# Kernel optimization log

Measured on AMD Instinct MI355X. Metric: run time of the kernel, lower is better.

Reference implementation:

```python
import jax, jax.numpy as jnp
import numpy as np

N = 13627
E = 504378
D = 500


def _seg_softmax(e, seg, n):
    m = jax.ops.segment_max(e, seg, num_segments=n)
    ex = jnp.exp(e - m[seg])
    s = jax.ops.segment_sum(ex, seg, num_segments=n)
    return ex / (s[seg] + 1e-16)


def _gatv2(x, src, dst, Wl, Wr, att, b, n):
    # PyG GATv2Conv (heads=1): message = Wl x_src; score uses Wl x_src + Wr x_dst
    xl = x @ Wl                                   # [N, F]
    xr = x @ Wr                                   # [N, F]
    e = jax.nn.leaky_relu(xl[src] + xr[dst], 0.2) @ att   # [E]
    a = _seg_softmax(e, dst, n)                   # segment softmax over targets
    out = jax.ops.segment_sum(a[:, None] * xl[src], dst, num_segments=n)
    return out + b


def setup_inputs() -> dict:
    key = jax.random.key(0)
    ks = jax.random.split(key, 24)
    s = 0.05
    inp = {
        'x': jax.random.normal(ks[0], (N, D), dtype=jnp.float32),
        'edge_index': jax.random.randint(ks[1], (2, E), 0, N),
        'neg_edge_index': jax.random.randint(ks[2], (2, E), 0, N),
        'Wl1': jax.random.normal(ks[3], (D, 300)) * s,
        'Wr1': jax.random.normal(ks[4], (D, 300)) * s,
        'att1': jax.random.normal(ks[5], (300,)) * s,
        'b1': jnp.zeros((300,)),
        'Wl2': jax.random.normal(ks[6], (300, 100)) * s,
        'Wr2': jax.random.normal(ks[7], (300, 100)) * s,
        'att2': jax.random.normal(ks[8], (100,)) * s,
        'b2': jnp.zeros((100,)),
        'Wl3': jax.random.normal(ks[9], (100, 1)) * s,
        'Wr3': jax.random.normal(ks[10], (100, 1)) * s,
        'att3': jax.random.normal(ks[11], (1,)) * s,
        'b3': jnp.zeros((1,)),
        'W_lin1': jax.random.normal(ks[12], (D, 100)) * s,
        'b_lin1': jnp.zeros((100,)),
        'W_lin2': jax.random.normal(ks[13], (D, 100)) * s,
        'b_lin2': jnp.zeros((100,)),
        'c1': jnp.array([0.5], dtype=jnp.float32),
        'c2': jnp.array([0.5], dtype=jnp.float32),
    }
    return inp


def reference(x, edge_index, neg_edge_index, Wl1, Wr1, att1, b1, Wl2, Wr2, att2, b2,
              Wl3, Wr3, att3, b3, W_lin1, b_lin1, W_lin2, b_lin2, c1, c2):
    # eval mode: dropout / dropout_adj are identity
    loops = jnp.arange(N)
    src = jnp.concatenate([edge_index[0], loops])   # GATv2Conv adds self loops
    dst = jnp.concatenate([edge_index[1], loops])

    h1 = jax.nn.relu(_gatv2(x, src, dst, Wl1, Wr1, att1, b1, N))
    h2 = jax.nn.relu(_gatv2(h1, src, dst, Wl2, Wr2, att2, b2, N))

    xo = h2 + jax.nn.relu(x @ W_lin1 + b_lin1)
    z = h2 + jax.nn.relu(x @ W_lin2 + b_lin2)

    # link-prediction reconstruction loss
    pos_s = jnp.sum(z[edge_index[0]] * z[edge_index[1]], axis=1)
    pos_loss = -jnp.mean(jnp.log(jax.nn.sigmoid(pos_s) + 1e-15))
    neg_s = jnp.sum(z[neg_edge_index[0]] * z[neg_edge_index[1]], axis=1)
    neg_loss = -jnp.mean(jnp.log(1.0 - jax.nn.sigmoid(neg_s) + 1e-15))
    r_loss = pos_loss + neg_loss

    out = _gatv2(xo, src, dst, Wl3, Wr3, att3, b3, N)   # [N, 1]
    return out, r_loss, c1, c2
```

## Files before the change

kernel.cpp:

```cpp
#include <hip/hip_runtime.h>
#include <hip/hip_bf16.h>

#define NODES 13627
#define DIM   500

typedef short short8 __attribute__((ext_vector_type(8)));
typedef float f32x4 __attribute__((ext_vector_type(4)));
typedef float floatx2 __attribute__((ext_vector_type(2)));

__device__ inline float wave_reduce_sum(float v) {
#pragma unroll
    for (int o = 32; o > 0; o >>= 1) v += __shfl_xor(v, o, 64);
    return v;
}

__device__ inline void store_v(float* p, float v) { *p = v; }
__device__ inline void store_v(__hip_bfloat16* p, float v) { *p = __float2bfloat16(v); }

__device__ inline float blo(unsigned w) { unsigned t = w << 16;        return __builtin_bit_cast(float, t); }
__device__ inline float bhi(unsigned w) { unsigned t = w & 0xffff0000u; return __builtin_bit_cast(float, t); }

__device__ inline unsigned char to_fp8(float v) {
    int r = __builtin_amdgcn_cvt_pk_fp8_f32(v, v, 0, false);
    return (unsigned char)(r & 0xff);
}

__device__ inline unsigned pk2bf(float a, float b) {
    unsigned la = (unsigned)__builtin_bit_cast(unsigned short, __float2bfloat16(a));
    unsigned hb = (unsigned)__builtin_bit_cast(unsigned short, __float2bfloat16(b));
    return la | (hb << 16);
}

struct b4 { __hip_bfloat16 a, b, c, d; };

__global__ __launch_bounds__(256) void hist_kernel(const int* __restrict__ dst,
                                                   int* __restrict__ cnt, int E) {
    int i = blockIdx.x * blockDim.x + threadIdx.x;
    if (i < E) atomicAdd(&cnt[dst[i]], 1);
}

__global__ __launch_bounds__(1024) void scan_kernel(int* __restrict__ cnt_cur,
                                                    int* __restrict__ off, int n) {
    __shared__ int wsum[16];
    const int tid = threadIdx.x, lane = tid & 63, w = tid >> 6;
    int carry = 0;
    for (int base = 0; base < n; base += 1024) {
        int i = base + tid;
        int v = (i < n) ? cnt_cur[i] : 0;
        int s = v;
#pragma unroll
        for (int o = 1; o < 64; o <<= 1) {
            int t = __shfl_up(s, o, 64);
            if (lane >= o) s += t;
        }
        if (lane == 63) wsum[w] = s;
        __syncthreads();
        if (w == 0 && lane < 16) {
            int x = wsum[lane];
            int sx = x;
#pragma unroll
            for (int o = 1; o < 16; o <<= 1) {
                int t = __shfl_up(sx, o, 64);
                if (lane >= o) sx += t;
            }
            wsum[lane] = sx;
        }
        __syncthreads();
        int wo = (w == 0) ? 0 : wsum[w - 1];
        int total = wsum[15];
        int excl = carry + wo + (s - v);
        if (i < n) { off[i] = excl; cnt_cur[i] = excl; }
        carry += total;
        __syncthreads();
    }
    if (tid == 0) off[n] = carry;
}

__global__ __launch_bounds__(256) void scatter_kernel(const int* __restrict__ src,
                                                      const int* __restrict__ dst,
                                                      int* __restrict__ cur,
                                                      int* __restrict__ ssrc, int E) {
    int i = blockIdx.x * blockDim.x + threadIdx.x;
    if (i < E) {
        int p = atomicAdd(&cur[dst[i]], 1);
        ssrc[p] = src[i];
    }
}

__global__ __launch_bounds__(256) void convert_all_kernel(
    const float* __restrict__ x,
    const float* __restrict__ Wl1, const float* __restrict__ Wr1,
    const float* __restrict__ Wl2, const float* __restrict__ Wr2,
    const float* __restrict__ Ws1, const float* __restrict__ Ws2,
    const float* __restrict__ bs1, const float* __restrict__ bs2,
    __hip_bfloat16* __restrict__ W1T, __hip_bfloat16* __restrict__ W2T,
    __hip_bfloat16* __restrict__ WsT, float* __restrict__ bcat,
    __hip_bfloat16* __restrict__ xb, int M) {
    int i = blockIdx.x * 256 + threadIdx.x;
    if (i < 327680) {
        int n = i >> 9, k = i & 511;
        float v = 0.f;
        if (k < 500) {
            if (n < 300) v = Wl1[k * 300 + n];
            else if (n < 600) v = Wr1[k * 300 + n - 300];
        }
        W1T[i] = __float2bfloat16(v);
    } else if (i < 409600) {
        int j = i - 327680;
        int n = j / 320, k = j - n * 320;
        float v = 0.f;
        if (k < 300) {
            if (n < 100) v = Wl2[k * 100 + n];
            else if (n < 200) v = Wr2[k * 100 + n - 100];
        }
        W2T[j] = __float2bfloat16(v);
    } else if (i < 540672) {
        int j = i - 409600;
        int n = j >> 9, k = j & 511;
        float v = 0.f;
        if (k < 500) {
            if (n < 100) v = Ws1[k * 100 + n];
            else if (n < 200) v = Ws2[k * 100 + n - 100];
        }
        WsT[j] = __float2bfloat16(v);
    } else if (i < 540928) {
        int n = i - 540672;
        float v = 0.f;
        if (n < 100) v = bs1[n];
        else if (n < 200) v = bs2[n - 100];
        bcat[n] = v;
    } else {
        int j = i - 540928;
        if (j >= M * 128) return;
        int m = j >> 7, k = (j & 127) << 2;
        b4 o;
        if (k < 500) {
            float4 v = *(const float4*)(x + (size_t)m * 500 + k);
            o.a = __float2bfloat16(v.x); o.b = __float2bfloat16(v.y);
            o.c = __float2bfloat16(v.z); o.d = __float2bfloat16(v.w);
        } else {
            o.a = o.b = o.c = o.d = __float2bfloat16(0.f);
        }
        *(b4*)(xb + (size_t)m * 512 + k) = o;
    }
}

template <int EPI, typename TC>
__global__ __launch_bounds__(256) void mfma_gemm(
    const __hip_bfloat16* __restrict__ A, const __hip_bfloat16* __restrict__ BT,
    TC* __restrict__ C, const float* __restrict__ bias, const float* __restrict__ h2,
    unsigned char* __restrict__ p8, __hip_bfloat16* __restrict__ pb,
    int M, int Kp, int Nn, int ldc) {
    __shared__ short AsF[8 * 64 * 8];
    __shared__ short BsF[4 * 64 * 8];
    const int t = threadIdx.x;
    const int w = t >> 6, lane = t & 63;
    const int c = t & 3, rr = t >> 2;
    const int m0 = blockIdx.y * 128, n0 = blockIdx.x * 64;

    f32x4 acc[2][4];
#pragma unroll
    for (int i = 0; i < 2; i++)
#pragma unroll
        for (int j = 0; j < 4; j++) acc[i][j] = (f32x4){0.f, 0.f, 0.f, 0.f};

    for (int k0 = 0; k0 < Kp; k0 += 32) {
#pragma unroll
        for (int r = 0; r < 2; r++) {
            int m = r * 64 + rr;
            int gm = m0 + m; if (gm >= M) gm = M - 1;
            float4 v = *(const float4*)(A + (size_t)gm * Kp + k0 + c * 8);
            int mi = m >> 4, sl = m & 15;
            *(float4*)(&AsF[(mi * 64 + c * 16 + sl) * 8]) = v;
        }
        {
            int n = rr;
            float4 v = *(const float4*)(BT + (size_t)(n0 + n) * Kp + k0 + c * 8);
            int ni = n >> 4, sl = n & 15;
            *(float4*)(&BsF[(ni * 64 + c * 16 + sl) * 8]) = v;
        }
        __syncthreads();
        short8 a0 = *(const short8*)(&AsF[((w * 2 + 0) * 64 + lane) * 8]);
        short8 a1 = *(const short8*)(&AsF[((w * 2 + 1) * 64 + lane) * 8]);
#pragma unroll
        for (int j = 0; j < 4; j++) {
            short8 b = *(const short8*)(&BsF[(j * 64 + lane) * 8]);
            acc[0][j] = __builtin_amdgcn_mfma_f32_16x16x32_bf16(a0, b, acc[0][j], 0, 0, 0);
            acc[1][j] = __builtin_amdgcn_mfma_f32_16x16x32_bf16(a1, b, acc[1][j], 0, 0, 0);
        }
        __syncthreads();
    }

    const int q = lane >> 4, sl = lane & 15;
#pragma unroll
    for (int i = 0; i < 2; i++) {
#pragma unroll
        for (int j = 0; j < 4; j++) {
#pragma unroll
            for (int reg = 0; reg < 4; reg++) {
                int gm = m0 + w * 32 + i * 16 + q * 4 + reg;
                int gn = n0 + j * 16 + sl;
                if (gm >= M) continue;
                float v = acc[i][j][reg];
                if constexpr (EPI == 1) {
                    if (gn < 300)       p8[(size_t)gm * 304 + gn] = to_fp8(v);
                    else if (gn < 600)  pb[(size_t)gm * 320 + (gn - 300)] = __float2bfloat16(v);
                    else if (gn < 620)  pb[(size_t)gm * 320 + (gn - 300)] = __float2bfloat16(0.f);
                    else if (gn < 624)  p8[(size_t)gm * 304 + (gn - 320)] = 0;
                } else if constexpr (EPI == 2) {
                    if (gn < 100)       p8[(size_t)gm * 112 + gn] = to_fp8(v);
                    else if (gn < 200)  pb[(size_t)gm * 128 + (gn - 100)] = __float2bfloat16(v);
                    else if (gn < 212)  p8[(size_t)gm * 112 + (gn - 100)] = 0;
                    else if (gn < 240)  pb[(size_t)gm * 128 + (gn - 112)] = __float2bfloat16(0.f);
                } else if constexpr (EPI == 3) {
                    if (gn < 200) {
                        int cn = gn < 100 ? gn : gn - 100;
                        float val = fmaxf(v + bias[gn], 0.f) + h2[(size_t)gm * 100 + cn];
                        if (gn < 100) C[(size_t)gm * 100 + gn] = val;
                        else p8[(size_t)gm * 128 + (gn - 100)] = to_fp8(val);
                    } else if (gn < 228) {
                        p8[(size_t)gm * 128 + (gn - 100)] = 0;
                    }
                } else {
                    store_v(&C[(size_t)gm * ldc + gn], v);
                }
            }
        }
    }
}

template <int F, int SL8, int SRB>
__global__ __launch_bounds__(256) void attdot_kernel(
    const unsigned char* __restrict__ xl8, const __hip_bfloat16* __restrict__ xrb,
    const float* __restrict__ att, float* __restrict__ sxl, float* __restrict__ sxr,
    int n) {
    const int wid = blockIdx.x * 4 + (threadIdx.x >> 6);
    const int lane = threadIdx.x & 63;
    if (wid >= n) return;
    float al = 0.f, ar = 0.f;
    for (int f0 = lane * 4; f0 < F; f0 += 256) {
        float4 a = *(const float4*)(att + f0);
        unsigned u = *(const unsigned*)(xl8 + (size_t)wid * SL8 + f0);
        floatx2 lo = __builtin_amdgcn_cvt_pk_f32_fp8((int)u, false);
        floatx2 hi = __builtin_amdgcn_cvt_pk_f32_fp8((int)u, true);
        al += a.x * lo.x + a.y * lo.y + a.z * hi.x + a.w * hi.y;
        uint2 r = *(const uint2*)(xrb + (size_t)wid * SRB + f0);
        ar += a.x * blo(r.x) + a.y * bhi(r.x) + a.z * blo(r.y) + a.w * bhi(r.y);
    }
    al = wave_reduce_sum(al);
    ar = wave_reduce_sum(ar);
    if (lane == 0) { sxl[wid] = 0.6f * al; sxr[wid] = 0.6f * ar; }
}

template <int F, int NJ, int SL8, int SRB, int SOUT, int JSL, typename TOUT>
__global__ __launch_bounds__(256) void gat_f8_kernel(
    const unsigned char* __restrict__ xl8, const __hip_bfloat16* __restrict__ xrb,
    const float* __restrict__ att, const float* __restrict__ bias,
    const float* __restrict__ sxl, const float* __restrict__ sxr,
    const int* __restrict__ off, const int* __restrict__ ssrc,
    TOUT* __restrict__ out, int n) {
    __shared__ float sden[2];
    __shared__ float sacc[2][NJ * 64];
    const int t = threadIdx.x;
    const int lane = t & 63;
    const int sl = lane & 15, q = lane >> 4;
    const int half = (t >> 6) & 1;
    const int pairIdx = t >> 7;
    int wid = blockIdx.x * 2 + pairIdx;
    if (wid >= n) wid = n - 1;

    float att4[NJ * 4], xrv[NJ * 4], acc[NJ * 4];
    const unsigned* xru = (const unsigned*)xrb + (size_t)wid * (SRB / 2);
#pragma unroll
    for (int j = 0; j < NJ; j++) {
        const int f0 = sl * 4 + j * 64;
        if (f0 < F) {
            float4 a4 = *(const float4*)(att + f0);
            att4[j * 4 + 0] = 0.4f * a4.x; att4[j * 4 + 1] = 0.4f * a4.y;
            att4[j * 4 + 2] = 0.4f * a4.z; att4[j * 4 + 3] = 0.4f * a4.w;
        } else {
            att4[j * 4 + 0] = att4[j * 4 + 1] = att4[j * 4 + 2] = att4[j * 4 + 3] = 0.f;
        }
        unsigned u0 = __builtin_nontemporal_load(xru + (f0 >> 1));
        unsigned u1 = __builtin_nontemporal_load(xru + (f0 >> 1) + 1);
        xrv[j * 4 + 0] = blo(u0); xrv[j * 4 + 1] = bhi(u0);
        xrv[j * 4 + 2] = blo(u1); xrv[j * 4 + 3] = bhi(u1);
        acc[j * 4 + 0] = acc[j * 4 + 1] = acc[j * 4 + 2] = acc[j * 4 + 3] = 0.f;
    }
    const float pbase = sxr[wid];

    const int s0 = off[wid], s1 = off[wid + 1];
    const int h0 = (s1 - s0) >> 1;
    const int eb = half ? (s0 + h0) : (s0 - 1);
    const int ee = half ? s1 : (s0 + h0);
    float den = 0.f;

    for (int e0 = eb; e0 < ee; e0 += 4) {
        const int eq = e0 + q;
        const bool act = eq < ee;
        int src = wid;
        if (act && eq >= s0) src = __builtin_nontemporal_load(ssrc + eq);
        const unsigned char* row = xl8 + (size_t)src * SL8;
        unsigned u[NJ];
#pragma unroll
        for (int j = 0; j < NJ; j++) {
            const bool ld = (j < NJ - 1) || (sl < JSL);
            u[j] = ld ? *(const unsigned*)(row + sl * 4 + j * 64) : 0u;
        }
        float xlv[NJ * 4];
        float p = (sl == 0) ? (pbase + sxl[src]) : 0.f;
#pragma unroll
        for (int j = 0; j < NJ; j++) {
            floatx2 lo = __builtin_amdgcn_cvt_pk_f32_fp8((int)u[j], false);
            floatx2 hi = __builtin_amdgcn_cvt_pk_f32_fp8((int)u[j], true);
            float v[4] = {lo.x, lo.y, hi.x, hi.y};
#pragma unroll
            for (int cc = 0; cc < 4; cc++) {
                xlv[j * 4 + cc] = v[cc];
                float s = v[cc] + xrv[j * 4 + cc];
                p = fmaf(att4[j * 4 + cc], fabsf(s), p);
            }
        }
        p += __shfl_xor(p, 1, 64);
        p += __shfl_xor(p, 2, 64);
        p += __shfl_xor(p, 4, 64);
        p += __shfl_xor(p, 8, 64);
        float ex = act ? expf(p) : 0.f;
        den += ex;
#pragma unroll
        for (int i = 0; i < NJ * 4; i++) acc[i] += ex * xlv[i];
    }

#pragma unroll
    for (int o = 16; o <= 32; o <<= 1) {
        den += __shfl_xor(den, o, 64);
#pragma unroll
        for (int i = 0; i < NJ * 4; i++) acc[i] += __shfl_xor(acc[i], o, 64);
    }

    if (half == 1 && lane < 16) {
        if (lane == 0) sden[pairIdx] = den;
#pragma unroll
        for (int j = 0; j < NJ; j++)
            *(float4*)(&sacc[pairIdx][sl * 4 + j * 64]) =
                make_float4(acc[j * 4 + 0], acc[j * 4 + 1], acc[j * 4 + 2], acc[j * 4 + 3]);
    }
    __syncthreads();
    if (half == 0 && lane < 16) {
        den += sden[pairIdx];
        const float inv = 1.f / (den + 1e-16f);
#pragma unroll
        for (int j = 0; j < NJ; j++) {
            const int f0 = sl * 4 + j * 64;
            if (f0 >= SOUT) continue;
            float4 o4 = *(float4*)(&sacc[pairIdx][f0]);
            float vv[4] = {acc[j * 4 + 0] + o4.x, acc[j * 4 + 1] + o4.y,
                           acc[j * 4 + 2] + o4.z, acc[j * 4 + 3] + o4.w};
            float r[4];
#pragma unroll
            for (int cc = 0; cc < 4; cc++) {
                const int f = f0 + cc;
                float v = 0.f;
                if (f < F) v = fmaxf(vv[cc] * inv + bias[f], 0.f);
                r[cc] = v;
            }
            if constexpr (sizeof(TOUT) == 4) {
                float* op = (float*)out + (size_t)wid * SOUT + f0;
                __builtin_nontemporal_store(r[0], op + 0);
                __builtin_nontemporal_store(r[1], op + 1);
                __builtin_nontemporal_store(r[2], op + 2);
                __builtin_nontemporal_store(r[3], op + 3);
            } else {
                unsigned* op = (unsigned*)out + (size_t)wid * (SOUT / 2) + (f0 >> 1);
                __builtin_nontemporal_store(pk2bf(r[0], r[1]), op);
                __builtin_nontemporal_store(pk2bf(r[2], r[3]), op + 1);
            }
        }
    }
}

__global__ __launch_bounds__(256) void gemm_vec1_kernel(
    const float* __restrict__ xo, const float* __restrict__ wl,
    const float* __restrict__ wr, float* __restrict__ xl3,
    float* __restrict__ xr3, int M, int ldx) {
    const int wid = blockIdx.x * 4 + (threadIdx.x >> 6);
    const int lane = threadIdx.x & 63;
    if (wid >= M) return;
    float a = 0.f, b = 0.f;
    for (int f = lane; f < 100; f += 64) {
        float v = xo[(size_t)wid * ldx + f];
        a += v * wl[f];
        b += v * wr[f];
    }
    a = wave_reduce_sum(a);
    b = wave_reduce_sum(b);
    if (lane == 0) { xl3[wid] = a; xr3[wid] = b; }
}

__global__ __launch_bounds__(256) void gat3_kernel(
    const float* __restrict__ xl3, const float* __restrict__ xr3,
    const float* __restrict__ att3, const float* __restrict__ b3,
    const int* __restrict__ off, const int* __restrict__ ssrc,
    float* __restrict__ out, int n) {
    const int wid = blockIdx.x * 4 + (threadIdx.x >> 6);
    const int lane = threadIdx.x & 63;
    if (wid >= n) return;
    const float xrv = xr3[wid];
    const float att = att3[0];
    float num = 0.f, den = 0.f;
    const int s0 = off[wid], s1 = off[wid + 1];
    for (int e = s0 - 1 + lane; e < s1; e += 64) {
        int src = (e < s0) ? wid : ssrc[e];
        float xlv = xl3[src];
        float t = xlv + xrv;
        float g = t > 0.f ? t : 0.2f * t;
        float ex = expf(g * att);
        den += ex;
        num += ex * xlv;
    }
    num = wave_reduce_sum(num);
    den = wave_reduce_sum(den);
    if (lane == 0) out[wid] = num / (den + 1e-16f) + b3[0];
}

__global__ __launch_bounds__(256) void loss_kernel(
    const unsigned char* __restrict__ z8, const int* __restrict__ pos,
    const int* __restrict__ neg, float* __restrict__ part, int nb, int E) {
    const int lane = threadIdx.x & 63;
    const int sl = lane & 15;
    const int wlocal = threadIdx.x >> 6;
    const int q = lane >> 4;
    const int nq = gridDim.x * 16;
    const int qid = (blockIdx.x * 4 + wlocal) * 4 + q;
    const int total = 2 * E;
    float psum = 0.f, nsum = 0.f;

    for (int base = qid; base < total; base += 4 * nq) {
        uint2 au[4], bu[4];
        bool act[4], isN[4];
#pragma unroll
        for (int s = 0; s < 4; s++) {
            int it = base + s * nq;
            act[s] = it < total;
            int itc = act[s] ? it : 0;
            isN[s] = itc >= E;
            int e = isN[s] ? itc - E : itc;
            const int* ei = isN[s] ? neg : pos;
            int u = ei[e], v = ei[E + e];
            au[s] = *(const uint2*)(z8 + (size_t)u * 128 + sl * 8);
            bu[s] = *(const uint2*)(z8 + (size_t)v * 128 + sl * 8);
        }
#pragma unroll
        for (int s = 0; s < 4; s++) {
            floatx2 a0 = __builtin_amdgcn_cvt_pk_f32_fp8((int)au[s].x, false);
            floatx2 a1 = __builtin_amdgcn_cvt_pk_f32_fp8((int)au[s].x, true);
            floatx2 a2 = __builtin_amdgcn_cvt_pk_f32_fp8((int)au[s].y, false);
            floatx2 a3 = __builtin_amdgcn_cvt_pk_f32_fp8((int)au[s].y, true);
            floatx2 b0 = __builtin_amdgcn_cvt_pk_f32_fp8((int)bu[s].x, false);
            floatx2 b1 = __builtin_amdgcn_cvt_pk_f32_fp8((int)bu[s].x, true);
            floatx2 b2 = __builtin_amdgcn_cvt_pk_f32_fp8((int)bu[s].y, false);
            floatx2 b3 = __builtin_amdgcn_cvt_pk_f32_fp8((int)bu[s].y, true);
            float p = a0.x * b0.x + a0.y * b0.y + a1.x * b1.x + a1.y * b1.y
                    + a2.x * b2.x + a2.y * b2.y + a3.x * b3.x + a3.y * b3.y;
            p += __shfl_xor(p, 1, 64);
            p += __shfl_xor(p, 2, 64);
            p += __shfl_xor(p, 4, 64);
            p += __shfl_xor(p, 8, 64);
            if (sl == 0 && act[s]) {
                float sig = 1.f / (1.f + expf(-p));
                if (isN[s]) nsum += logf(1.f - sig + 1e-15f);
                else        psum += logf(sig + 1e-15f);
            }
        }
    }
    float pw = wave_reduce_sum(psum);
    float nw = wave_reduce_sum(nsum);
    __shared__ float sp[4], sn[4];
    if (lane == 0) { sp[wlocal] = pw; sn[wlocal] = nw; }
    __syncthreads();
    if (threadIdx.x == 0) {
        part[blockIdx.x]      = sp[0] + sp[1] + sp[2] + sp[3];
        part[nb + blockIdx.x] = sn[0] + sn[1] + sn[2] + sn[3];
    }
}

__global__ __launch_bounds__(1024) void finalize_kernel(
    const float* __restrict__ part, int nb,
    const float* __restrict__ c1, const float* __restrict__ c2,
    float* __restrict__ out, int n, int E) {
    __shared__ float sp[16], sn[16];
    const int tid = threadIdx.x, lane = tid & 63, w = tid >> 6;
    float p = 0.f, q = 0.f;
    for (int i = tid; i < nb; i += 1024) { p += part[i]; q += part[nb + i]; }
    p = wave_reduce_sum(p);
    q = wave_reduce_sum(q);
    if (lane == 0) { sp[w] = p; sn[w] = q; }
    __syncthreads();
    if (tid == 0) {
        float tp = 0.f, tq = 0.f;
#pragma unroll
        for (int i = 0; i < 16; i++) { tp += sp[i]; tq += sn[i]; }
        out[n]     = -(tp + tq) / (float)E;
        out[n + 1] = c1[0];
        out[n + 2] = c2[0];
    }
}

extern "C" void kernel_launch(void* const* d_in, const int* in_sizes, int n_in,
                              void* d_out, int out_size, void* d_ws, size_t ws_size,
                              hipStream_t stream) {
    const float* x      = (const float*)d_in[0];
    const int*   ei     = (const int*)d_in[1];
    const int*   nei    = (const int*)d_in[2];
    const float* Wl1    = (const float*)d_in[3];
    const float* Wr1    = (const float*)d_in[4];
    const float* att1   = (const float*)d_in[5];
    const float* b1     = (const float*)d_in[6];
    const float* Wl2    = (const float*)d_in[7];
    const float* Wr2    = (const float*)d_in[8];
    const float* att2   = (const float*)d_in[9];
    const float* b2     = (const float*)d_in[10];
    const float* Wl3    = (const float*)d_in[11];
    const float* Wr3    = (const float*)d_in[12];
    const float* att3   = (const float*)d_in[13];
    const float* b3     = (const float*)d_in[14];
    const float* Wlin1  = (const float*)d_in[15];
    const float* blin1  = (const float*)d_in[16];
    const float* Wlin2  = (const float*)d_in[17];
    const float* blin2  = (const float*)d_in[18];
    const float* c1     = (const float*)d_in[19];
    const float* c2     = (const float*)d_in[20];
    float* out = (float*)d_out;

    const int E = in_sizes[1] / 2;
    const int N = NODES;
    const int LOSS_BLOCKS = 4096;

    char* ws = (char*)d_ws;
    unsigned char*  xl8  = (unsigned char*)(ws + 0);
    unsigned char*  xl28 = (unsigned char*)(ws + 0);
    __hip_bfloat16* xrb  = (__hip_bfloat16*)(ws + 4194304);
    __hip_bfloat16* xr2b = (__hip_bfloat16*)(ws + 4194304);
    float*          xo   = (float*)(ws + 4194304);
    unsigned char*  z8   = (unsigned char*)(ws + 9645312);
    __hip_bfloat16* h1b  = (__hip_bfloat16*)(ws + 12915712);
    float*          h2   = (float*)(ws + 12915712);
    __hip_bfloat16* xb   = (__hip_bfloat16*)(ws + 21637120);
    __hip_bfloat16* W1T  = (__hip_bfloat16*)(ws + 35591168);
    __hip_bfloat16* W2T  = (__hip_bfloat16*)(ws + 36246528);
    __hip_bfloat16* WsT  = (__hip_bfloat16*)(ws + 36410368);
    float*          bcat = (float*)(ws + 36672512);
    float*          xl3  = (float*)(ws + 36673536);
    float*          xr3  = (float*)(ws + 36728064);
    int*            ioff = (int*)(ws + 36782592);
    int*            cur  = (int*)(ws + 36837376);
    int*            ssrc = (int*)(ws + 36892160);
    float*          part = (float*)(ws + 38909952);
    float*          sxl  = (float*)(ws + 38942720);
    float*          sxr  = (float*)(ws + 38997248);

    hipMemsetAsync(cur, 0, sizeof(int) * N, stream);

    hist_kernel<<<(E + 255) / 256, 256, 0, stream>>>(ei + E, cur, E);
    scan_kernel<<<1, 1024, 0, stream>>>(cur, ioff, N);
    scatter_kernel<<<(E + 255) / 256, 256, 0, stream>>>(ei, ei + E, cur, ssrc, E);

    convert_all_kernel<<<(540928 + N * 128 + 255) / 256, 256, 0, stream>>>(
        x, Wl1, Wr1, Wl2, Wr2, Wlin1, Wlin2, blin1, blin2,
        W1T, W2T, WsT, bcat, xb, N);

    mfma_gemm<1, __hip_bfloat16><<<dim3(10, 107), 256, 0, stream>>>(
        xb, W1T, (__hip_bfloat16*)nullptr, nullptr, nullptr, xl8, xrb, N, 512, 640, 0);
    attdot_kernel<300, 304, 320><<<(N + 3) / 4, 256, 0, stream>>>(
        xl8, xrb, att1, sxl, sxr, N);
    gat_f8_kernel<300, 5, 304, 320, 320, 11, __hip_bfloat16>
        <<<(N + 1) / 2, 256, 0, stream>>>(xl8, xrb, att1, b1, sxl, sxr, ioff, ssrc, h1b, N);

    mfma_gemm<2, __hip_bfloat16><<<dim3(4, 107), 256, 0, stream>>>(
        h1b, W2T, (__hip_bfloat16*)nullptr, nullptr, nullptr, xl28, xr2b, N, 320, 256, 0);
    attdot_kernel<100, 112, 128><<<(N + 3) / 4, 256, 0, stream>>>(
        xl28, xr2b, att2, sxl, sxr, N);
    gat_f8_kernel<100, 2, 112, 128, 100, 9, float>
        <<<(N + 1) / 2, 256, 0, stream>>>(xl28, xr2b, att2, b2, sxl, sxr, ioff, ssrc, h2, N);

    mfma_gemm<3, float><<<dim3(4, 107), 256, 0, stream>>>(
        xb, WsT, xo, bcat, h2, z8, nullptr, N, 512, 256, 0);

    loss_kernel<<<LOSS_BLOCKS, 256, 0, stream>>>(z8, ei, nei, part, LOSS_BLOCKS, E);

    gemm_vec1_kernel<<<(N + 3) / 4, 256, 0, stream>>>(xo, Wl3, Wr3, xl3, xr3, N, 100);
    gat3_kernel<<<(N + 3) / 4, 256, 0, stream>>>(xl3, xr3, att3, b3, ioff, ssrc, out, N);

    finalize_kernel<<<1, 1024, 0, stream>>>(part, LOSS_BLOCKS, c1, c2, out, N, E);
}
```

Measured before the change: 408.3 us.

## Drop attdot precompute, compute leaky-relu directly, and prefetch next edge rows in GAT

Removes the two attdot kernels. Before, leaky_relu was split into a linear part (0.6·att·x, precomputed per node) plus 0.4·att·|s|. Now the full leaky_relu is evaluated in-loop with fmax(s, 0.2s), which saves two launches and the per-edge sxl gather. The edge loop is software-pipelined: the next group's source index and fp8 row are loaded before the current one is processed, to hide gather latency. The cost is more registers per thread. Nontemporal output stores become plain or vectorised stores.

```diff
diff --git a/kernel.cpp b/kernel.cpp
--- a/kernel.cpp
+++ b/kernel.cpp
@@ -229,34 +229,10 @@
     }
 }
 
-template <int F, int SL8, int SRB>
-__global__ __launch_bounds__(256) void attdot_kernel(
-    const unsigned char* __restrict__ xl8, const __hip_bfloat16* __restrict__ xrb,
-    const float* __restrict__ att, float* __restrict__ sxl, float* __restrict__ sxr,
-    int n) {
-    const int wid = blockIdx.x * 4 + (threadIdx.x >> 6);
-    const int lane = threadIdx.x & 63;
-    if (wid >= n) return;
-    float al = 0.f, ar = 0.f;
-    for (int f0 = lane * 4; f0 < F; f0 += 256) {
-        float4 a = *(const float4*)(att + f0);
-        unsigned u = *(const unsigned*)(xl8 + (size_t)wid * SL8 + f0);
-        floatx2 lo = __builtin_amdgcn_cvt_pk_f32_fp8((int)u, false);
-        floatx2 hi = __builtin_amdgcn_cvt_pk_f32_fp8((int)u, true);
-        al += a.x * lo.x + a.y * lo.y + a.z * hi.x + a.w * hi.y;
-        uint2 r = *(const uint2*)(xrb + (size_t)wid * SRB + f0);
-        ar += a.x * blo(r.x) + a.y * bhi(r.x) + a.z * blo(r.y) + a.w * bhi(r.y);
-    }
-    al = wave_reduce_sum(al);
-    ar = wave_reduce_sum(ar);
-    if (lane == 0) { sxl[wid] = 0.6f * al; sxr[wid] = 0.6f * ar; }
-}
-
 template <int F, int NJ, int SL8, int SRB, int SOUT, int JSL, typename TOUT>
 __global__ __launch_bounds__(256) void gat_f8_kernel(
     const unsigned char* __restrict__ xl8, const __hip_bfloat16* __restrict__ xrb,
     const float* __restrict__ att, const float* __restrict__ bias,
-    const float* __restrict__ sxl, const float* __restrict__ sxr,
     const int* __restrict__ off, const int* __restrict__ ssrc,
     TOUT* __restrict__ out, int n) {
     __shared__ float sden[2];
@@ -269,17 +245,17 @@
     int wid = blockIdx.x * 2 + pairIdx;
     if (wid >= n) wid = n - 1;
 
-    float att4[NJ * 4], xrv[NJ * 4], acc[NJ * 4];
+    float attv[NJ * 4], xrv[NJ * 4], acc[NJ * 4];
     const unsigned* xru = (const unsigned*)xrb + (size_t)wid * (SRB / 2);
 #pragma unroll
     for (int j = 0; j < NJ; j++) {
         const int f0 = sl * 4 + j * 64;
         if (f0 < F) {
             float4 a4 = *(const float4*)(att + f0);
-            att4[j * 4 + 0] = 0.4f * a4.x; att4[j * 4 + 1] = 0.4f * a4.y;
-            att4[j * 4 + 2] = 0.4f * a4.z; att4[j * 4 + 3] = 0.4f * a4.w;
+            attv[j * 4 + 0] = a4.x; attv[j * 4 + 1] = a4.y;
+            attv[j * 4 + 2] = a4.z; attv[j * 4 + 3] = a4.w;
         } else {
-            att4[j * 4 + 0] = att4[j * 4 + 1] = att4[j * 4 + 2] = att4[j * 4 + 3] = 0.f;
+            attv[j * 4 + 0] = attv[j * 4 + 1] = attv[j * 4 + 2] = attv[j * 4 + 3] = 0.f;
         }
         unsigned u0 = __builtin_nontemporal_load(xru + (f0 >> 1));
         unsigned u1 = __builtin_nontemporal_load(xru + (f0 >> 1) + 1);
@@ -287,7 +263,6 @@
         xrv[j * 4 + 2] = blo(u1); xrv[j * 4 + 3] = bhi(u1);
         acc[j * 4 + 0] = acc[j * 4 + 1] = acc[j * 4 + 2] = acc[j * 4 + 3] = 0.f;
     }
-    const float pbase = sxr[wid];
 
     const int s0 = off[wid], s1 = off[wid + 1];
     const int h0 = (s1 - s0) >> 1;
@@ -295,20 +270,35 @@
     const int ee = half ? s1 : (s0 + h0);
     float den = 0.f;
 
-    for (int e0 = eb; e0 < ee; e0 += 4) {
-        const int eq = e0 + q;
-        const bool act = eq < ee;
+    unsigned u[NJ];
+    {
+        int eq = eb + q;
         int src = wid;
-        if (act && eq >= s0) src = __builtin_nontemporal_load(ssrc + eq);
+        if (eq >= s0 && eq < ee) src = __builtin_nontemporal_load(ssrc + eq);
         const unsigned char* row = xl8 + (size_t)src * SL8;
-        unsigned u[NJ];
 #pragma unroll
         for (int j = 0; j < NJ; j++) {
             const bool ld = (j < NJ - 1) || (sl < JSL);
             u[j] = ld ? *(const unsigned*)(row + sl * 4 + j * 64) : 0u;
         }
+    }
+
+    for (int e0 = eb; e0 < ee; e0 += 4) {
+        const bool act = (e0 + q) < ee;
+        unsigned un[NJ];
+        {
+            int eq1 = e0 + 4 + q;
+            int src1 = wid;
+            if (eq1 >= s0 && eq1 < ee) src1 = __builtin_nontemporal_load(ssrc + eq1);
+            const unsigned char* row1 = xl8 + (size_t)src1 * SL8;
+#pragma unroll
+            for (int j = 0; j < NJ; j++) {
+                const bool ld = (j < NJ - 1) || (sl < JSL);
+                un[j] = ld ? *(const unsigned*)(row1 + sl * 4 + j * 64) : 0u;
+            }
+        }
         float xlv[NJ * 4];
-        float p = (sl == 0) ? (pbase + sxl[src]) : 0.f;
+        float p = 0.f;
 #pragma unroll
         for (int j = 0; j < NJ; j++) {
             floatx2 lo = __builtin_amdgcn_cvt_pk_f32_fp8((int)u[j], false);
@@ -318,7 +308,7 @@
             for (int cc = 0; cc < 4; cc++) {
                 xlv[j * 4 + cc] = v[cc];
                 float s = v[cc] + xrv[j * 4 + cc];
-                p = fmaf(att4[j * 4 + cc], fabsf(s), p);
+                p += attv[j * 4 + cc] * fmaxf(s, 0.2f * s);
             }
         }
         p += __shfl_xor(p, 1, 64);
@@ -329,6 +319,8 @@
         den += ex;
 #pragma unroll
         for (int i = 0; i < NJ * 4; i++) acc[i] += ex * xlv[i];
+#pragma unroll
+        for (int j = 0; j < NJ; j++) u[j] = un[j];
     }
 
 #pragma unroll
@@ -365,15 +357,12 @@
                 r[cc] = v;
             }
             if constexpr (sizeof(TOUT) == 4) {
-                float* op = (float*)out + (size_t)wid * SOUT + f0;
-                __builtin_nontemporal_store(r[0], op + 0);
-                __builtin_nontemporal_store(r[1], op + 1);
-                __builtin_nontemporal_store(r[2], op + 2);
-                __builtin_nontemporal_store(r[3], op + 3);
+                *(float4*)((float*)out + (size_t)wid * SOUT + f0) =
+                    make_float4(r[0], r[1], r[2], r[3]);
             } else {
                 unsigned* op = (unsigned*)out + (size_t)wid * (SOUT / 2) + (f0 >> 1);
-                __builtin_nontemporal_store(pk2bf(r[0], r[1]), op);
-                __builtin_nontemporal_store(pk2bf(r[2], r[3]), op + 1);
+                op[0] = pk2bf(r[0], r[1]);
+                op[1] = pk2bf(r[2], r[3]);
             }
         }
     }
@@ -556,8 +545,6 @@
     int*            cur  = (int*)(ws + 36837376);
     int*            ssrc = (int*)(ws + 36892160);
     float*          part = (float*)(ws + 38909952);
-    float*          sxl  = (float*)(ws + 38942720);
-    float*          sxr  = (float*)(ws + 38997248);
 
     hipMemsetAsync(cur, 0, sizeof(int) * N, stream);
 
@@ -571,17 +558,13 @@
 
     mfma_gemm<1, __hip_bfloat16><<<dim3(10, 107), 256, 0, stream>>>(
         xb, W1T, (__hip_bfloat16*)nullptr, nullptr, nullptr, xl8, xrb, N, 512, 640, 0);
-    attdot_kernel<300, 304, 320><<<(N + 3) / 4, 256, 0, stream>>>(
-        xl8, xrb, att1, sxl, sxr, N);
     gat_f8_kernel<300, 5, 304, 320, 320, 11, __hip_bfloat16>
-        <<<(N + 1) / 2, 256, 0, stream>>>(xl8, xrb, att1, b1, sxl, sxr, ioff, ssrc, h1b, N);
+        <<<(N + 1) / 2, 256, 0, stream>>>(xl8, xrb, att1, b1, ioff, ssrc, h1b, N);
 
     mfma_gemm<2, __hip_bfloat16><<<dim3(4, 107), 256, 0, stream>>>(
         h1b, W2T, (__hip_bfloat16*)nullptr, nullptr, nullptr, xl28, xr2b, N, 320, 256, 0);
-    attdot_kernel<100, 112, 128><<<(N + 3) / 4, 256, 0, stream>>>(
-        xl28, xr2b, att2, sxl, sxr, N);
     gat_f8_kernel<100, 2, 112, 128, 100, 9, float>
-        <<<(N + 1) / 2, 256, 0, stream>>>(xl28, xr2b, att2, b2, sxl, sxr, ioff, ssrc, h2, N);
+        <<<(N + 1) / 2, 256, 0, stream>>>(xl28, xr2b, att2, b2, ioff, ssrc, h2, N);
 
     mfma_gemm<3, float><<<dim3(4, 107), 256, 0, stream>>>(
         xb, WsT, xo, bcat, h2, z8, nullptr, N, 512, 256, 0);
```

Measured after the change: 390.4 us. 1.05x faster.
